# Kernel optimization log

Hardware: AMD Instinct MI355X
Metric: run time of the kernel (lower is better)

## Reference

```python
import jax, jax.numpy as jnp
import numpy as np

N_NODES = 100_000
SCALAR_DIM = 64
HIDDEN = 64
ATTR_DIM = 3
N_DIH = 1_000_000
IN_DIM = SCALAR_DIM * 2 + ATTR_DIM + 2  # 133
EPS_LN = 1e-5
EPS_NORM = 1e-6


def setup_inputs() -> dict:
    key = jax.random.key(0)
    ks = jax.random.split(key, 8)
    x = jax.random.normal(ks[0], (N_NODES, SCALAR_DIM), jnp.float32)
    pos = jax.random.normal(ks[1], (N_NODES, 3), jnp.float32)
    quadra_index = jax.random.randint(ks[2], (4, N_DIH), 0, N_NODES, jnp.int32)
    quadra_attr = jax.random.normal(ks[3], (N_DIH, ATTR_DIM), jnp.float32)

    def lin(k, fi, fo):
        lim = 1.0 / np.sqrt(fi)
        return jax.random.uniform(k, (fi, fo), jnp.float32, -lim, lim)

    return dict(
        x=x, pos=pos, quadra_index=quadra_index, quadra_attr=quadra_attr,
        ln_gamma=jnp.ones((IN_DIM,), jnp.float32),
        ln_beta=jnp.zeros((IN_DIM,), jnp.float32),
        w1=lin(ks[4], IN_DIM, HIDDEN), b1=jnp.zeros((HIDDEN,), jnp.float32),
        w2=lin(ks[5], HIDDEN, HIDDEN), b2=jnp.zeros((HIDDEN,), jnp.float32),
        w3=lin(ks[6], HIDDEN, SCALAR_DIM), b3=jnp.zeros((SCALAR_DIM,), jnp.float32),
        w_out=jax.random.normal(ks[7], (SCALAR_DIM, SCALAR_DIM), jnp.float32),
    )


def _dihedral_cos_sin(pos, i, j, k, l):
    b1 = pos[j] - pos[i]
    b2 = pos[k] - pos[j]
    b3 = pos[l] - pos[k]
    n1 = jnp.cross(b1, b2)
    n2 = jnp.cross(b2, b3)
    n1 = n1 / jnp.maximum(jnp.linalg.norm(n1, axis=-1, keepdims=True), EPS_NORM)
    n2 = n2 / jnp.maximum(jnp.linalg.norm(n2, axis=-1, keepdims=True), EPS_NORM)
    cos_d = jnp.clip(jnp.sum(n1 * n2, axis=-1), -1.0, 1.0)
    b2n = b2 / jnp.maximum(jnp.linalg.norm(b2, axis=-1, keepdims=True), EPS_NORM)
    m = jnp.cross(n1, b2n)
    sin_d = jnp.sum(m * n2, axis=-1)
    return cos_d, sin_d


def _segment_mean(v, idx, n):
    s = jax.ops.segment_sum(v, idx, num_segments=n)
    c = jax.ops.segment_sum(jnp.ones((idx.shape[0], 1), v.dtype), idx, num_segments=n)
    return s / jnp.maximum(c, 1.0)


def reference(x, pos, quadra_index, quadra_attr,
              ln_gamma, ln_beta, w1, b1, w2, b2, w3, b3, w_out):
    i, j, k, l = quadra_index[0], quadra_index[1], quadra_index[2], quadra_index[3]
    x_scalar = x[:, :SCALAR_DIM]
    cos_d, sin_d = _dihedral_cos_sin(pos, i, j, k, l)
    # [num_dihedrals, 2*scalar_dim + 3 + 2]
    inp = jnp.concatenate(
        [x_scalar[i], x_scalar[l], quadra_attr, cos_d[:, None], sin_d[:, None]], axis=-1)
    # LayerNorm over last dim
    mu = jnp.mean(inp, axis=-1, keepdims=True)
    var = jnp.mean(jnp.square(inp - mu), axis=-1, keepdims=True)
    inp = (inp - mu) * jax.lax.rsqrt(var + EPS_LN) * ln_gamma + ln_beta
    # MLP with SiLU
    h = jax.nn.silu(inp @ w1 + b1)
    h = jax.nn.silu(h @ w2 + b2)
    msg = h @ w3 + b3  # [num_dihedrals, scalar_dim]
    aggr = 0.5 * (_segment_mean(msg, j, N_NODES) + _segment_mean(msg, k, N_NODES))
    # e3nn o3.Linear on scalars: fan-in normalized linear, no bias
    out = (aggr @ w_out) * (1.0 / np.sqrt(SCALAR_DIM))
    return out
```

## Files before the change

kernel.cpp:

```cpp
#include <hip/hip_runtime.h>
#include <math.h>

#define NN 100000
#define ND 1000000
#define INDIM 133
#define K1P 160
#define NCNT (2*NN)
#define SCAN_CHUNK 2048
#define NBLK_SCAN ((NCNT + SCAN_CHUNK - 1) / SCAN_CHUNK)
#define HS 72
#define NBLK_X (NN / 4)
#define NBLK_E ((ND + 255) / 256)

typedef __bf16 bf16x8 __attribute__((ext_vector_type(8)));
typedef __bf16 bf16x4 __attribute__((ext_vector_type(4)));
typedef float  f32x4  __attribute__((ext_vector_type(4)));
typedef _Float16 f16;
typedef _Float16 f16x4 __attribute__((ext_vector_type(4)));

__device__ __forceinline__ f32x4 mfma_bf16(bf16x8 a, bf16x8 b, f32x4 c) {
    return __builtin_amdgcn_mfma_f32_16x16x32_bf16(a, b, c, 0, 0, 0);
}

__device__ __forceinline__ float3 f3sub(float3 a, float3 b) {
    return make_float3(a.x - b.x, a.y - b.y, a.z - b.z);
}
__device__ __forceinline__ float3 f3cross(float3 a, float3 b) {
    return make_float3(a.y * b.z - a.z * b.y, a.z * b.x - a.x * b.z, a.x * b.y - a.y * b.x);
}
__device__ __forceinline__ float f3dot(float3 a, float3 b) {
    return a.x * b.x + a.y * b.y + a.z * b.z;
}
__device__ __forceinline__ float3 f3load(const float* __restrict__ p, int idx) {
    const float* q = p + (size_t)idx * 3;
    return make_float3(q[0], q[1], q[2]);
}
__device__ __forceinline__ float fsilu(float v) {
    return v / (1.0f + __expf(-v));
}

__global__ __launch_bounds__(256) void prep_merged(
    const float* __restrict__ x,
    const float* __restrict__ w1, const float* __restrict__ b1,
    const float* __restrict__ w2,
    const float* __restrict__ w3, const float* __restrict__ b3,
    const float* __restrict__ wout,
    const float* __restrict__ gamma, const float* __restrict__ beta,
    const int* __restrict__ qidx,
    __bf16* __restrict__ w1h, __bf16* __restrict__ w1l,
    float* __restrict__ c1, float* __restrict__ d1,
    __bf16* __restrict__ w2h, __bf16* __restrict__ w2l,
    __bf16* __restrict__ w3h, __bf16* __restrict__ w3l,
    float* __restrict__ b3f,
    float2* __restrict__ sq,
    int* __restrict__ cnt)
{
    const int b = blockIdx.x, tid = threadIdx.x;
    if (b < 40) {
        int idx = b * 256 + tid;
        int n = idx / K1P, kp = idx - n * K1P;
        float v = (kp < INDIM) ? gamma[kp] * w1[(size_t)kp * 64 + n] : 0.0f;
        __bf16 h = (__bf16)v;
        w1h[idx] = h;
        w1l[idx] = (__bf16)(v - (float)h);
    } else if (b == 40) {
        if (tid < 64) {
            float sc = 0.0f, sd = 0.0f;
            for (int k = 0; k < INDIM; ++k) {
                float wv = w1[(size_t)k * 64 + tid];
                sc = fmaf(gamma[k], wv, sc);
                sd = fmaf(beta[k], wv, sd);
            }
            c1[tid] = sc;
            d1[tid] = sd + b1[tid];
        }
    } else if (b < 57) {
        int idx = (b - 41) * 256 + tid;
        int n = idx >> 6, kp = idx & 63;
        int ko = 16 * (kp & 3) + (kp >> 2);
        float v = w2[(size_t)ko * 64 + n];
        __bf16 h = (__bf16)v;
        w2h[idx] = h;
        w2l[idx] = (__bf16)(v - (float)h);
    } else if (b == 57) {
        for (int idx = tid; idx < 64 * 64; idx += 256) {
            int k = idx >> 6, c = idx & 63;
            float s = 0.0f;
            for (int q = 0; q < 64; ++q)
                s = fmaf(w3[(size_t)k * 64 + q], wout[(size_t)q * 64 + c], s);
            s *= 0.0625f;
            __bf16 h = (__bf16)s;
            int kp = 4 * (k & 15) + (k >> 4);
            w3h[(size_t)c * 64 + kp] = h;
            w3l[(size_t)c * 64 + kp] = (__bf16)(s - (float)h);
        }
        if (tid < 64) {
            float s = 0.0f;
            for (int q = 0; q < 64; ++q)
                s = fmaf(b3[q], wout[(size_t)q * 64 + tid], s);
            b3f[tid] = s * 0.0625f;
        }
    } else if (b < 58 + NBLK_X) {
        const int n = (b - 58) * 4 + (tid >> 6);
        const int c = tid & 63;
        float v = x[(size_t)n * 64 + c];
        float s = v, q = v * v;
#pragma unroll
        for (int d = 1; d < 64; d <<= 1) {
            s += __shfl_xor(s, d);
            q += __shfl_xor(q, d);
        }
        if (c == 0) sq[n] = make_float2(s, q);
    } else {
        int e = (b - 58 - NBLK_X) * 256 + tid;
        if (e < ND) {
            atomicAdd(&cnt[qidx[ND + e]], 1);
            atomicAdd(&cnt[NN + qidx[2 * ND + e]], 1);
        }
    }
}

__global__ __launch_bounds__(256) void scan1(int* data, int* __restrict__ bsum) {
    __shared__ int lds[256];
    const int tid = threadIdx.x;
    const int base = blockIdx.x * SCAN_CHUNK + tid * 8;
    int v[8];
    int tsum = 0;
#pragma unroll
    for (int t = 0; t < 8; ++t) {
        v[t] = (base + t < NCNT) ? data[base + t] : 0;
        tsum += v[t];
    }
    lds[tid] = tsum;
    __syncthreads();
    for (int d = 1; d < 256; d <<= 1) {
        int u = 0;
        if (tid >= d) u = lds[tid - d];
        __syncthreads();
        lds[tid] += u;
        __syncthreads();
    }
    if (tid == 255) bsum[blockIdx.x] = lds[255];
    int run = lds[tid] - tsum;
#pragma unroll
    for (int t = 0; t < 8; ++t) {
        if (base + t < NCNT) data[base + t] = run;
        run += v[t];
    }
}

__global__ __launch_bounds__(128) void scan2(int* __restrict__ bsum) {
    __shared__ int lds[128];
    const int t = threadIdx.x;
    int v = (t < NBLK_SCAN) ? bsum[t] : 0;
    lds[t] = v;
    __syncthreads();
    for (int d = 1; d < 128; d <<= 1) {
        int u = (t >= d) ? lds[t - d] : 0;
        __syncthreads();
        lds[t] += u;
        __syncthreads();
    }
    if (t < NBLK_SCAN) bsum[t] = lds[t] - v;
}

__global__ __launch_bounds__(256) void scan3(int* __restrict__ off,
                                             const int* __restrict__ bsum) {
    const int base = blockIdx.x * SCAN_CHUNK + threadIdx.x * 8;
    const int add = bsum[blockIdx.x];
#pragma unroll
    for (int t = 0; t < 8; ++t) {
        int i = base + t;
        if (i < NCNT) off[i] += add;
    }
}

__global__ __launch_bounds__(256) void fill_kernel(const int* __restrict__ qidx,
                                                   int* __restrict__ off,
                                                   int* __restrict__ slot_j,
                                                   int* __restrict__ slot_k) {
    int e = blockIdx.x * 256 + threadIdx.x;
    if (e < ND) {
        slot_j[e] = atomicAdd(&off[qidx[ND + e]], 1);
        slot_k[e] = atomicAdd(&off[NN + qidx[2 * ND + e]], 1);
    }
}

__global__ __launch_bounds__(256, 4) void edge_mlp_mfma(
    const float* __restrict__ x,
    const float2* __restrict__ sq,
    const float* __restrict__ pos,
    const int* __restrict__ qidx, const float* __restrict__ qattr,
    const __bf16* __restrict__ w1h, const __bf16* __restrict__ w1l,
    const float* __restrict__ c1, const float* __restrict__ d1,
    const __bf16* __restrict__ w2h, const __bf16* __restrict__ w2l, const float* __restrict__ b2,
    const __bf16* __restrict__ w3h, const __bf16* __restrict__ w3l, const float* __restrict__ b3f,
    const int* __restrict__ slot_j, const int* __restrict__ slot_k,
    f16* __restrict__ msg)
{
    __shared__ __align__(16) __bf16 hsh[4][16 * HS];

    const int tid = threadIdx.x;
    const int w   = tid >> 6;
    const int l   = tid & 63;
    const int m   = l & 15;
    const int kg  = l >> 4;
    const int ebase = (blockIdx.x * 4 + w) * 64;
    if (ebase >= ND) return;

    int iA[4], lA[4];
#pragma unroll
    for (int t = 0; t < 4; ++t) {
        const int e = ebase + 16 * t + m;
        iA[t] = qidx[e];
        lA[t] = qidx[3 * ND + e];
    }

    float cosd, sind, at0, at1, at2, se, qe;
    {
        const int e2 = ebase + 16 * kg + m;
        const int i2 = qidx[e2];
        const int j2 = qidx[ND + e2];
        const int k2 = qidx[2 * ND + e2];
        const int l2 = qidx[3 * ND + e2];
        float3 pi = f3load(pos, i2), pj = f3load(pos, j2);
        float3 pk = f3load(pos, k2), pl = f3load(pos, l2);
        float3 d1v_ = f3sub(pj, pi);
        float3 d2v_ = f3sub(pk, pj);
        float3 d3v_ = f3sub(pl, pk);
        float3 n1 = f3cross(d1v_, d2v_);
        float3 n2 = f3cross(d2v_, d3v_);
        float r1 = 1.0f / fmaxf(sqrtf(f3dot(n1, n1)), 1e-6f);
        n1.x *= r1; n1.y *= r1; n1.z *= r1;
        float r2 = 1.0f / fmaxf(sqrtf(f3dot(n2, n2)), 1e-6f);
        n2.x *= r2; n2.y *= r2; n2.z *= r2;
        cosd = fminf(fmaxf(f3dot(n1, n2), -1.0f), 1.0f);
        float rb = 1.0f / fmaxf(sqrtf(f3dot(d2v_, d2v_)), 1e-6f);
        float3 b2n = make_float3(d2v_.x * rb, d2v_.y * rb, d2v_.z * rb);
        float3 mm = f3cross(n1, b2n);
        sind = f3dot(mm, n2);
        at0 = qattr[(size_t)e2 * 3 + 0];
        at1 = qattr[(size_t)e2 * 3 + 1];
        at2 = qattr[(size_t)e2 * 3 + 2];
        se = at0 + at1 + at2 + cosd + sind;
        qe = at0 * at0 + at1 * at1 + at2 * at2 + cosd * cosd + sind * sind;
    }

    bf16x8 ah4[4], al4[4];
    float rs_[4], mn_[4];
#pragma unroll
    for (int t = 0; t < 4; ++t) {
        const int src = m + 16 * t;
        float u4[8] = {__shfl(at0, src), __shfl(at1, src), __shfl(at2, src),
                       __shfl(cosd, src), __shfl(sind, src), 0.f, 0.f, 0.f};
        float g0 = (kg == 0) ? 1.0f : 0.0f;
#pragma unroll
        for (int j = 0; j < 8; ++j) {
            float v = u4[j] * g0;
            __bf16 h = (__bf16)v;
            ah4[t][j] = h;
            al4[t][j] = (__bf16)(v - (float)h);
        }
        float2 si = sq[iA[t]], sl = sq[lA[t]];
        float S = si.x + sl.x + __shfl(se, src);
        float Q = si.y + sl.y + __shfl(qe, src);
        float mu  = S * (1.0f / INDIM);
        float var = Q * (1.0f / INDIM) - mu * mu;
        float rsv = rsqrtf(fmaxf(var, 0.0f) + 1e-5f);
        rs_[t] = rsv;
        mn_[t] = -mu * rsv;
    }

    f32x4 acc[4][4];
#pragma unroll
    for (int t = 0; t < 4; ++t)
#pragma unroll
        for (int nt = 0; nt < 4; ++nt) acc[t][nt] = (f32x4){0.f, 0.f, 0.f, 0.f};

#pragma unroll
    for (int nt = 0; nt < 4; ++nt) {
        const size_t wb = (size_t)(16 * nt + m) * K1P + 128 + 8 * kg;
        bf16x8 bh = *(const bf16x8*)(w1h + wb);
        bf16x8 bl = *(const bf16x8*)(w1l + wb);
#pragma unroll
        for (int t = 0; t < 4; ++t) {
            acc[t][nt] = mfma_bf16(ah4[t], bh, acc[t][nt]);
            acc[t][nt] = mfma_bf16(al4[t], bh, acc[t][nt]);
            acc[t][nt] = mfma_bf16(ah4[t], bl, acc[t][nt]);
        }
    }

#pragma unroll
    for (int s = 0; s < 4; ++s) {
        const int colo = 32 * (s & 1) + 8 * kg;
        bf16x8 ath[4], atl[4];
#pragma unroll
        for (int t = 0; t < 4; ++t) {
            const int r_ = (s < 2) ? iA[t] : lA[t];
            float vv[8];
            *(float4*)&vv[0] = *(const float4*)(x + (size_t)r_ * 64 + colo);
            *(float4*)&vv[4] = *(const float4*)(x + (size_t)r_ * 64 + colo + 4);
#pragma unroll
            for (int j = 0; j < 8; ++j) {
                float v = vv[j];
                __bf16 h = (__bf16)v;
                ath[t][j] = h;
                atl[t][j] = (__bf16)(v - (float)h);
            }
        }
#pragma unroll
        for (int nt = 0; nt < 4; ++nt) {
            const size_t wb = (size_t)(16 * nt + m) * K1P + 32 * s + 8 * kg;
            bf16x8 bh = *(const bf16x8*)(w1h + wb);
            bf16x8 bl = *(const bf16x8*)(w1l + wb);
#pragma unroll
            for (int t = 0; t < 4; ++t) {
                acc[t][nt] = mfma_bf16(ath[t], bh, acc[t][nt]);
                acc[t][nt] = mfma_bf16(atl[t], bh, acc[t][nt]);
                acc[t][nt] = mfma_bf16(ath[t], bl, acc[t][nt]);
            }
        }
    }

    float c1v[4], d1v[4], b2v[4], b3v[4];
#pragma unroll
    for (int nt = 0; nt < 4; ++nt) {
        c1v[nt] = c1[16 * nt + m];
        d1v[nt] = d1[16 * nt + m];
        b2v[nt] = b2[16 * nt + m];
        b3v[nt] = b3f[16 * nt + m];
    }
    __bf16* hhw = &hsh[w][0];
    bf16x8 a2h[4][2];
#pragma unroll
    for (int t = 0; t < 4; ++t) {
#pragma unroll
        for (int r = 0; r < 4; ++r) {
            float rse = __shfl(rs_[t], 4 * kg + r);
            float mne = __shfl(mn_[t], 4 * kg + r);
            bf16x4 hv4;
#pragma unroll
            for (int nt = 0; nt < 4; ++nt)
                hv4[nt] = (__bf16)fsilu(fmaf(rse, acc[t][nt][r],
                                        fmaf(mne, c1v[nt], d1v[nt])));
            *(bf16x4*)(hhw + (4 * kg + r) * HS + m * 4) = hv4;
        }
#pragma unroll
        for (int s = 0; s < 2; ++s)
            a2h[t][s] = *(const bf16x8*)(hhw + m * HS + 32 * s + 8 * kg);
    }

    f32x4 acc2[4][4];
#pragma unroll
    for (int t = 0; t < 4; ++t)
#pragma unroll
        for (int nt = 0; nt < 4; ++nt) acc2[t][nt] = (f32x4){0.f, 0.f, 0.f, 0.f};
#pragma unroll
    for (int s = 0; s < 2; ++s) {
#pragma unroll
        for (int nt = 0; nt < 4; ++nt) {
            const size_t wb = (size_t)(16 * nt + m) * 64 + 32 * s + 8 * kg;
            bf16x8 bh = *(const bf16x8*)(w2h + wb);
            bf16x8 bl = *(const bf16x8*)(w2l + wb);
#pragma unroll
            for (int t = 0; t < 4; ++t) {
                acc2[t][nt] = mfma_bf16(a2h[t][s], bh, acc2[t][nt]);
                acc2[t][nt] = mfma_bf16(a2h[t][s], bl, acc2[t][nt]);
            }
        }
    }

    bf16x8 a3h[4][2];
#pragma unroll
    for (int t = 0; t < 4; ++t) {
#pragma unroll
        for (int r = 0; r < 4; ++r) {
            bf16x4 hv4;
#pragma unroll
            for (int nt = 0; nt < 4; ++nt)
                hv4[nt] = (__bf16)fsilu(acc2[t][nt][r] + b2v[nt]);
            *(bf16x4*)(hhw + (4 * kg + r) * HS + m * 4) = hv4;
        }
#pragma unroll
        for (int s = 0; s < 2; ++s)
            a3h[t][s] = *(const bf16x8*)(hhw + m * HS + 32 * s + 8 * kg);
    }

    f32x4 acc3[4][4];
#pragma unroll
    for (int t = 0; t < 4; ++t)
#pragma unroll
        for (int nt = 0; nt < 4; ++nt) acc3[t][nt] = (f32x4){0.f, 0.f, 0.f, 0.f};
#pragma unroll
    for (int s = 0; s < 2; ++s) {
#pragma unroll
        for (int nt = 0; nt < 4; ++nt) {
            const size_t wb = (size_t)(16 * nt + m) * 64 + 32 * s + 8 * kg;
            bf16x8 bh = *(const bf16x8*)(w3h + wb);
            bf16x8 bl = *(const bf16x8*)(w3l + wb);
#pragma unroll
            for (int t = 0; t < 4; ++t) {
                acc3[t][nt] = mfma_bf16(a3h[t][s], bh, acc3[t][nt]);
                acc3[t][nt] = mfma_bf16(a3h[t][s], bl, acc3[t][nt]);
            }
        }
    }

#pragma unroll
    for (int t = 0; t < 4; ++t) {
#pragma unroll
        for (int r = 0; r < 4; ++r) {
            f16x4 v;
#pragma unroll
            for (int nt = 0; nt < 4; ++nt)
                v[nt] = (f16)(acc3[t][nt][r] + b3v[nt]);
            const int er = ebase + 16 * t + 4 * kg + r;
            *(f16x4*)(msg + (size_t)slot_j[er] * 64 + m * 4) = v;
            *(f16x4*)(msg + (size_t)slot_k[er] * 64 + m * 4) = v;
        }
    }
}

__global__ __launch_bounds__(256) void node_out(const f16* __restrict__ msg,
                                                const int* __restrict__ off,
                                                float* __restrict__ out) {
    const int w   = threadIdx.x >> 6;
    const int l   = threadIdx.x & 63;
    const int sub = l >> 4;
    const int m16 = l & 15;
    for (int n = blockIdx.x * 4 + w; n < NN; n += gridDim.x * 4) {
        int ja = (n == 0) ? 0 : off[n - 1];
        int jb = off[n];
        int ka = off[NN + n - 1];
        int kb = off[NN + n];
        float s0 = 0.f, s1 = 0.f, s2 = 0.f, s3 = 0.f;
        float t0 = 0.f, t1 = 0.f, t2 = 0.f, t3 = 0.f;
        for (int p = ja + sub; p < jb; p += 4) {
            f16x4 v = *(const f16x4*)(msg + (size_t)p * 64 + m16 * 4);
            s0 += (float)v[0]; s1 += (float)v[1];
            s2 += (float)v[2]; s3 += (float)v[3];
        }
        for (int p = ka + sub; p < kb; p += 4) {
            f16x4 v = *(const f16x4*)(msg + (size_t)p * 64 + m16 * 4);
            t0 += (float)v[0]; t1 += (float)v[1];
            t2 += (float)v[2]; t3 += (float)v[3];
        }
        s0 += __shfl_xor(s0, 16); s0 += __shfl_xor(s0, 32);
        s1 += __shfl_xor(s1, 16); s1 += __shfl_xor(s1, 32);
        s2 += __shfl_xor(s2, 16); s2 += __shfl_xor(s2, 32);
        s3 += __shfl_xor(s3, 16); s3 += __shfl_xor(s3, 32);
        t0 += __shfl_xor(t0, 16); t0 += __shfl_xor(t0, 32);
        t1 += __shfl_xor(t1, 16); t1 += __shfl_xor(t1, 32);
        t2 += __shfl_xor(t2, 16); t2 += __shfl_xor(t2, 32);
        t3 += __shfl_xor(t3, 16); t3 += __shfl_xor(t3, 32);
        if (sub == 0) {
            float rj = 1.0f / fmaxf((float)(jb - ja), 1.0f);
            float rk = 1.0f / fmaxf((float)(kb - ka), 1.0f);
            float* o = out + (size_t)n * 64;
            o[m16]      = s0 * rj + t0 * rk;
            o[16 + m16] = s1 * rj + t1 * rk;
            o[32 + m16] = s2 * rj + t2 * rk;
            o[48 + m16] = s3 * rj + t3 * rk;
        }
    }
}


extern "C" void kernel_launch(void* const* d_in, const int* in_sizes, int n_in,
                              void* d_out, int out_size, void* d_ws, size_t ws_size,
                              hipStream_t stream) {
    (void)in_sizes; (void)n_in; (void)out_size;

    const float* x     = (const float*)d_in[0];
    const float* pos   = (const float*)d_in[1];
    const int*   qidx  = (const int*)d_in[2];
    const float* qattr = (const float*)d_in[3];
    const float* gamma = (const float*)d_in[4];
    const float* beta  = (const float*)d_in[5];
    const float* w1    = (const float*)d_in[6];
    const float* b1    = (const float*)d_in[7];
    const float* w2    = (const float*)d_in[8];
    const float* b2    = (const float*)d_in[9];
    const float* w3    = (const float*)d_in[10];
    const float* b3    = (const float*)d_in[11];
    const float* w_out = (const float*)d_in[12];
    float* out = (float*)d_out;

    size_t o = 0;
    auto alloc = [&](size_t bytes) { size_t r = o; o = (o + bytes + 255) & ~(size_t)255; return r; };
    char* W = (char*)d_ws;
    f16*    msg    = (f16*)   (W + alloc((size_t)2 * ND * 64 * sizeof(f16)));
    int*    slot_j = (int*)   (W + alloc((size_t)ND * sizeof(int)));
    int*    slot_k = (int*)   (W + alloc((size_t)ND * sizeof(int)));
    int*    off    = (int*)   (W + alloc((size_t)NCNT * sizeof(int)));
    int*    bsum   = (int*)   (W + alloc((size_t)NBLK_SCAN * sizeof(int)));
    float2* sqt    = (float2*)(W + alloc((size_t)NN * sizeof(float2)));
    __bf16* w1h    = (__bf16*)(W + alloc((size_t)64 * K1P * sizeof(__bf16)));
    __bf16* w1l    = (__bf16*)(W + alloc((size_t)64 * K1P * sizeof(__bf16)));
    __bf16* w2h    = (__bf16*)(W + alloc((size_t)64 * 64 * sizeof(__bf16)));
    __bf16* w2l    = (__bf16*)(W + alloc((size_t)64 * 64 * sizeof(__bf16)));
    __bf16* w3h    = (__bf16*)(W + alloc((size_t)64 * 64 * sizeof(__bf16)));
    __bf16* w3l    = (__bf16*)(W + alloc((size_t)64 * 64 * sizeof(__bf16)));
    float*  c1     = (float*) (W + alloc((size_t)64 * sizeof(float)));
    float*  d1     = (float*) (W + alloc((size_t)64 * sizeof(float)));
    float*  b3f    = (float*) (W + alloc((size_t)64 * sizeof(float)));
    if (ws_size < o) return;

    hipMemsetAsync(off, 0, (size_t)NCNT * sizeof(int), stream);
    prep_merged<<<58 + NBLK_X + NBLK_E, 256, 0, stream>>>(
        x, w1, b1, w2, w3, b3, w_out, gamma, beta, qidx,
        w1h, w1l, c1, d1, w2h, w2l, w3h, w3l, b3f, sqt, off);

    scan1<<<NBLK_SCAN, 256, 0, stream>>>(off, bsum);
    scan2<<<1, 128, 0, stream>>>(bsum);
    scan3<<<NBLK_SCAN, 256, 0, stream>>>(off, bsum);
    fill_kernel<<<NBLK_E, 256, 0, stream>>>(qidx, off, slot_j, slot_k);

    edge_mlp_mfma<<<(ND / 64 + 3) / 4, 256, 0, stream>>>(
        x, sqt, pos, qidx, qattr, w1h, w1l, c1, d1,
        w2h, w2l, b2, w3h, w3l, b3f, slot_j, slot_k, msg);

    node_out<<<4096, 256, 0, stream>>>(msg, off, out);
}
```

Measured before the change: 556.4 us.

## Fuse slot-claiming atomics into edge MLP kernel and remove fill kernel

The separate fill kernel that claimed CSR slots with atomics, and the slot_j/slot_k arrays it wrote, are removed. Each wave now does the atomicAdd on the offsets at the start of the edge MLP kernel and shuffles the resulting slots to the lanes that scatter messages. The LDS staging buffer is widened to one tile per t, so all four tiles are written before any are read back, and the launch bound drops from 4 to 3 blocks per CU. This saves a kernel launch and a round trip of the slot arrays through memory, at the cost of more LDS, lower occupancy, and atomic latency inside the compute kernel.

```diff
diff --git a/kernel.cpp b/kernel.cpp
--- a/kernel.cpp
+++ b/kernel.cpp
@@ -175,18 +175,7 @@
     }
 }
 
-__global__ __launch_bounds__(256) void fill_kernel(const int* __restrict__ qidx,
-                                                   int* __restrict__ off,
-                                                   int* __restrict__ slot_j,
-                                                   int* __restrict__ slot_k) {
-    int e = blockIdx.x * 256 + threadIdx.x;
-    if (e < ND) {
-        slot_j[e] = atomicAdd(&off[qidx[ND + e]], 1);
-        slot_k[e] = atomicAdd(&off[NN + qidx[2 * ND + e]], 1);
-    }
-}
-
-__global__ __launch_bounds__(256, 4) void edge_mlp_mfma(
+__global__ __launch_bounds__(256, 3) void edge_mlp_mfma(
     const float* __restrict__ x,
     const float2* __restrict__ sq,
     const float* __restrict__ pos,
@@ -195,10 +184,10 @@
     const float* __restrict__ c1, const float* __restrict__ d1,
     const __bf16* __restrict__ w2h, const __bf16* __restrict__ w2l, const float* __restrict__ b2,
     const __bf16* __restrict__ w3h, const __bf16* __restrict__ w3l, const float* __restrict__ b3f,
-    const int* __restrict__ slot_j, const int* __restrict__ slot_k,
+    int* __restrict__ off,
     f16* __restrict__ msg)
 {
-    __shared__ __align__(16) __bf16 hsh[4][16 * HS];
+    __shared__ __align__(16) __bf16 hsh[4][4][16 * HS];
 
     const int tid = threadIdx.x;
     const int w   = tid >> 6;
@@ -207,6 +196,13 @@
     const int kg  = l >> 4;
     const int ebase = (blockIdx.x * 4 + w) * 64;
     if (ebase >= ND) return;
+
+    int vj, vk;
+    {
+        const int me = ebase + l;
+        vj = atomicAdd(&off[qidx[ND + me]], 1);
+        vk = atomicAdd(&off[NN + qidx[2 * ND + me]], 1);
+    }
 
     int iA[4], lA[4];
 #pragma unroll
@@ -330,10 +326,9 @@
         b2v[nt] = b2[16 * nt + m];
         b3v[nt] = b3f[16 * nt + m];
     }
-    __bf16* hhw = &hsh[w][0];
-    bf16x8 a2h[4][2];
 #pragma unroll
     for (int t = 0; t < 4; ++t) {
+        __bf16* hhw = &hsh[w][t][0];
 #pragma unroll
         for (int r = 0; r < 4; ++r) {
             float rse = __shfl(rs_[t], 4 * kg + r);
@@ -345,11 +340,14 @@
                                         fmaf(mne, c1v[nt], d1v[nt])));
             *(bf16x4*)(hhw + (4 * kg + r) * HS + m * 4) = hv4;
         }
+    }
+
+    bf16x8 a2h[4][2];
+#pragma unroll
+    for (int t = 0; t < 4; ++t)
 #pragma unroll
         for (int s = 0; s < 2; ++s)
-            a2h[t][s] = *(const bf16x8*)(hhw + m * HS + 32 * s + 8 * kg);
-    }
-
+            a2h[t][s] = *(const bf16x8*)(&hsh[w][t][m * HS + 32 * s + 8 * kg]);
     f32x4 acc2[4][4];
 #pragma unroll
     for (int t = 0; t < 4; ++t)
@@ -369,10 +367,9 @@
             }
         }
     }
-
-    bf16x8 a3h[4][2];
 #pragma unroll
     for (int t = 0; t < 4; ++t) {
+        __bf16* hhw = &hsh[w][t][0];
 #pragma unroll
         for (int r = 0; r < 4; ++r) {
             bf16x4 hv4;
@@ -381,11 +378,14 @@
                 hv4[nt] = (__bf16)fsilu(acc2[t][nt][r] + b2v[nt]);
             *(bf16x4*)(hhw + (4 * kg + r) * HS + m * 4) = hv4;
         }
+    }
+
+    bf16x8 a3h[4][2];
+#pragma unroll
+    for (int t = 0; t < 4; ++t)
 #pragma unroll
         for (int s = 0; s < 2; ++s)
-            a3h[t][s] = *(const bf16x8*)(hhw + m * HS + 32 * s + 8 * kg);
-    }
-
+            a3h[t][s] = *(const bf16x8*)(&hsh[w][t][m * HS + 32 * s + 8 * kg]);
     f32x4 acc3[4][4];
 #pragma unroll
     for (int t = 0; t < 4; ++t)
@@ -414,9 +414,11 @@
 #pragma unroll
             for (int nt = 0; nt < 4; ++nt)
                 v[nt] = (f16)(acc3[t][nt][r] + b3v[nt]);
-            const int er = ebase + 16 * t + 4 * kg + r;
-            *(f16x4*)(msg + (size_t)slot_j[er] * 64 + m * 4) = v;
-            *(f16x4*)(msg + (size_t)slot_k[er] * 64 + m * 4) = v;
+            const int src = 16 * t + 4 * kg + r;
+            const int sjv = __shfl(vj, src);
+            const int skv = __shfl(vk, src);
+            *(f16x4*)(msg + (size_t)sjv * 64 + m * 4) = v;
+            *(f16x4*)(msg + (size_t)skv * 64 + m * 4) = v;
         }
     }
 }
@@ -490,8 +492,6 @@
     auto alloc = [&](size_t bytes) { size_t r = o; o = (o + bytes + 255) & ~(size_t)255; return r; };
     char* W = (char*)d_ws;
     f16*    msg    = (f16*)   (W + alloc((size_t)2 * ND * 64 * sizeof(f16)));
-    int*    slot_j = (int*)   (W + alloc((size_t)ND * sizeof(int)));
-    int*    slot_k = (int*)   (W + alloc((size_t)ND * sizeof(int)));
     int*    off    = (int*)   (W + alloc((size_t)NCNT * sizeof(int)));
     int*    bsum   = (int*)   (W + alloc((size_t)NBLK_SCAN * sizeof(int)));
     float2* sqt    = (float2*)(W + alloc((size_t)NN * sizeof(float2)));
@@ -514,11 +514,10 @@
     scan1<<<NBLK_SCAN, 256, 0, stream>>>(off, bsum);
     scan2<<<1, 128, 0, stream>>>(bsum);
     scan3<<<NBLK_SCAN, 256, 0, stream>>>(off, bsum);
-    fill_kernel<<<NBLK_E, 256, 0, stream>>>(qidx, off, slot_j, slot_k);
 
     edge_mlp_mfma<<<(ND / 64 + 3) / 4, 256, 0, stream>>>(
         x, sqt, pos, qidx, qattr, w1h, w1l, c1, d1,
-        w2h, w2l, b2, w3h, w3l, b3f, slot_j, slot_k, msg);
+        w2h, w2l, b2, w3h, w3l, b3f, off, msg);
 
     node_out<<<4096, 256, 0, stream>>>(msg, off, out);
 }
```

Result: faster. 487.7 us (median of 2 runs) (-12.4%).
